# Performance work log

Hardware: AMD Instinct MI355X
Metric: run time of the kernel (lower is better)

## Reference

```python
import jax, jax.numpy as jnp
import numpy as np

D, T1, T2, T3 = 1024, 256, 128, 64
IV2, IV3, BUF = 16, 128, 32
B, T = 16, 1024

_PARAM_SHAPES = {
    "w_t1g": (D + T1, T1), "b_t1g": (T1,),
    "w_t1c": (D + T1, T1), "b_t1c": (T1,),
    "w_t1r": (T1, D), "b_t1r": (D,),
    "w_t2v": (D, T2), "b_t2v": (T2,),
    "w_t2b": (D, 1), "b_t2b": (1,),
    "w_t2r": (T2, D), "b_t2r": (D,),
    "w_t3o": (D, T3), "b_t3o": (T3,),
    "w_t3n": (D, T3), "b_t3n": (T3,),
    "w_t3r": (2 * T3, D), "b_t3r": (D,),
    "w_b32": (T3, T2), "b_b32": (T2,),
    "w_b21": (T2, T1), "b_b21": (T1,),
    "w_fuse": (3 * D, D), "b_fuse": (D,),
}

def setup_inputs() -> dict:
    key = jax.random.key(0)
    inp = {"x": jax.random.normal(jax.random.fold_in(key, 0), (B, T, D), jnp.float32)}
    for i, (name, shape) in enumerate(_PARAM_SHAPES.items()):
        inp[name] = 0.02 * jax.random.normal(jax.random.fold_in(key, i + 1), shape, jnp.float32)
    inp["ln_g"] = jnp.ones((D,), jnp.float32)
    inp["ln_b"] = jnp.zeros((D,), jnp.float32)
    return inp

def reference(x, w_t1g, b_t1g, w_t1c, b_t1c, w_t1r, b_t1r, w_t2v, b_t2v, w_t2b, b_t2b, w_t2r, b_t2r, w_t3o, b_t3o, w_t3n, b_t3n, w_t3r, b_t3r, w_b32, b_b32, w_b21, b_b21, w_fuse, b_fuse, ln_g, ln_b):
    Bsz, Tlen, _ = x.shape
    tier1 = jnp.zeros((Bsz, T1), x.dtype)
    tier2 = jnp.zeros((Bsz, T2), x.dtype)
    tier3 = jnp.zeros((Bsz, T3), x.dtype)
    var3 = jnp.ones((Bsz, T3), x.dtype)
    buf = jnp.zeros((Bsz, BUF, D), x.dtype)  # consolidation buffer

    def step(carry, inp_t):
        tier1, tier2, tier3, var3, buf = carry
        x_t, tc = inp_t  # tc = token_count (1-indexed)
        # cross-tier broadcasts
        bias21 = jnp.tanh(tier2 @ w_b21 + b_b21)
        bias32 = jnp.tanh(tier3 @ w_b32 + b_b32)
        # tier1: GRU-style gated update
        t1b = tier1 + bias21
        comb = jnp.concatenate([x_t, t1b], axis=-1)
        gate = jax.nn.sigmoid(comb @ w_t1g + b_t1g)
        cand = jnp.tanh(comb @ w_t1c + b_t1c)
        tier1 = gate * t1b + (1.0 - gate) * cand
        read1 = tier1 @ w_t1r + b_t1r
        # tier2: delta-rule overwrite every IV2 tokens (buffer mean BEFORE this token is written)
        do2 = (tc % IV2) == 0
        bm = buf.mean(axis=1)
        t2b = tier2 + bias32
        v = bm @ w_t2v + b_t2v
        beta = jax.nn.sigmoid(bm @ w_t2b + b_t2b)
        tier2 = jnp.where(do2, t2b + beta * (v - t2b), tier2)
        read2 = tier2 @ w_t2r + b_t2r
        # tier3: diagonal Kalman update every IV3 tokens, observation = tier2 readout
        do3 = (tc % IV3) == 0
        z = read2 @ w_t3o + b_t3o
        r = jax.nn.softplus(read2 @ w_t3n + b_t3n) + 0.01
        sp = 0.99 * var3 + 0.01
        K = sp / (sp + r + 1e-8)
        tier3 = jnp.where(do3, tier3 + K * (z - tier3), tier3)
        var3 = jnp.where(do3, (1.0 - K) * sp, var3)
        read3 = jnp.concatenate([tier3, var3], axis=-1) @ w_t3r + b_t3r
        fused = jnp.concatenate([read1, read2, read3], axis=-1) @ w_fuse + b_fuse
        # ring-buffer write (detached in torch -> stop_gradient)
        idx = (tc - 1) % BUF
        buf = jax.lax.dynamic_update_slice(buf, jax.lax.stop_gradient(x_t)[:, None, :], (0, idx, 0))
        return (tier1, tier2, tier3, var3, buf), fused

    tcs = jnp.arange(1, Tlen + 1, dtype=jnp.int32)
    _, ys = jax.lax.scan(step, (tier1, tier2, tier3, var3, buf), (jnp.swapaxes(x, 0, 1), tcs))
    out = jnp.swapaxes(ys, 0, 1)  # [B, T, D]
    mu = out.mean(-1, keepdims=True)
    xc = out - mu
    return xc * jax.lax.rsqrt(jnp.mean(xc * xc, -1, keepdims=True) + 1e-5) * ln_g + ln_b
```

## Files before the change

### kernel.cpp

```cpp
#include <hip/hip_runtime.h>

#define D_ 1024
#define T_ 1024
#define B_ 16

typedef short s16x8 __attribute__((ext_vector_type(8)));
typedef float f32x4 __attribute__((ext_vector_type(4)));

__device__ __forceinline__ unsigned short bf16_rne(float f){
  unsigned int u = __builtin_bit_cast(unsigned int, f);
  u += 0x7FFFu + ((u >> 16) & 1u);
  return (unsigned short)(u >> 16);
}
__device__ __forceinline__ float bf16_tof(unsigned short h){
  unsigned int u = ((unsigned int)h) << 16;
  return __builtin_bit_cast(float, u);
}
__device__ __forceinline__ float fsig(float x){ return 1.0f/(1.0f+__expf(-x)); }
__device__ __forceinline__ float ftanh(float x){ return 2.0f*fsig(2.0f*x)-1.0f; }

template <typename V>
__device__ __forceinline__ auto mfma_try(V a, V b, f32x4 c, int)
    -> decltype(__builtin_amdgcn_mfma_f32_16x16x32_bf16(a, b, c, 0, 0, 0)) {
  return __builtin_amdgcn_mfma_f32_16x16x32_bf16(a, b, c, 0, 0, 0);
}
template <typename V>
__device__ __forceinline__ f32x4 mfma_try(V a, V b, f32x4 c, long) {
  typedef __bf16 bf16x8 __attribute__((ext_vector_type(8)));
  return __builtin_amdgcn_mfma_f32_16x16x32_bf16(
      __builtin_bit_cast(bf16x8, a), __builtin_bit_cast(bf16x8, b), c, 0, 0, 0);
}
__device__ __forceinline__ f32x4 MFMA(s16x8 a, s16x8 b, f32x4 c){
  return mfma_try(a, b, c, 0);
}


__device__ __forceinline__ void dev_conv4(const float* __restrict__ s,
                                          unsigned short* __restrict__ d, int g){
  float4 v = *(const float4*)(s + (size_t)g*4);
  ushort4 o; o.x=bf16_rne(v.x); o.y=bf16_rne(v.y); o.z=bf16_rne(v.z); o.w=bf16_rne(v.w);
  *(ushort4*)(d + (size_t)g*4) = o;
}

__device__ __forceinline__ void dev_fragprep(const float* __restrict__ w, int rowOff,
                                             int KT, int Nsrc,
                                             unsigned short* __restrict__ dst, int slot){
  int lane = slot & 63; int tmp = slot >> 6; int kt = tmp % KT; int nt = tmp / KT;
  int kbase = kt*32 + (lane>>4)*8; int col = nt*16 + (lane&15);
  unsigned short* o = dst + (size_t)slot*8;
  #pragma unroll
  for (int j=0;j<8;j++) o[j] = bf16_rne(w[(size_t)(rowOff + kbase + j)*Nsrc + col]);
}

__device__ __forceinline__ void dev_bm(const float* __restrict__ x,
                                       unsigned short* __restrict__ bm, int blk, int tid){
  int e = blk >> 4; int b = blk & 15;
  int tc = 16*(e+1); int hi = tc-2; int lo = tc-33; if (lo < 0) lo = 0;
  const float* xb = x + (size_t)b*T_*D_;
  for (int d = tid; d < D_; d += 256){
    float s = 0.f;
    for (int ss = lo; ss <= hi; ++ss) s += xb[(size_t)ss*D_ + d];
    bm[((size_t)(e*16+b))*D_ + d] = bf16_rne(s * (1.0f/32.0f));
  }
}

__device__ __forceinline__ void dev_bconst(const float* __restrict__ wf, const float* __restrict__ bf,
                                           const float* __restrict__ b1, const float* __restrict__ b2,
                                           const float* __restrict__ b3, float* __restrict__ bc,
                                           int blk, int tid){
  __shared__ float part[4][64];
  int n = blk*64 + (tid&63);
  int sl = tid>>6;
  float s = 0.f;
  for (int k=sl*256; k<(sl+1)*256; ++k){
    s += b1[k]*wf[(size_t)k*1024+n] + b2[k]*wf[(size_t)(1024+k)*1024+n] + b3[k]*wf[(size_t)(2048+k)*1024+n];
  }
  part[sl][tid&63] = s; __syncthreads();
  if (sl==0) bc[n] = bf[n] + part[0][tid] + part[1][tid] + part[2][tid] + part[3][tid];
}

__device__ __forceinline__ void dev_b2(const float* __restrict__ b_t2r, const float* __restrict__ w3o,
                                       const float* __restrict__ b3o, const float* __restrict__ w3n,
                                       const float* __restrict__ b3n, float* __restrict__ b2o,
                                       float* __restrict__ b2n, int tid){
  __shared__ float part[2][128];
  int idx = tid & 127; int sl = tid >> 7;
  int mat = idx>>6, n = idx&63;
  const float* w = mat ? w3n : w3o;
  float s = 0.f;
  for (int k=sl*512; k<(sl+1)*512; ++k) s += b_t2r[k]*w[(size_t)k*64+n];
  part[sl][idx] = s; __syncthreads();
  if (sl==0){
    float r = part[0][idx] + part[1][idx] + (mat? b3n[n] : b3o[n]);
    if (mat) b2n[n] = r; else b2o[n] = r;
  }
}

__device__ __forceinline__ void dev_gemm(int M, int K,
    const unsigned short* __restrict__ A, int lda,
    const unsigned short* __restrict__ Bf,
    const float* __restrict__ bias, int act,
    float* __restrict__ C, int ldc, int cb, int rb, int tid, int rows){
  int KT = K >> 5;
  int w = tid >> 6, l = tid & 63;
  int rbase = rb*rows + w*16;
  int arow = rbase + (l & 15); if (arow >= M) arow = M-1;
  const unsigned short* Aptr = A + (size_t)arow*lda + ((l>>4)*8);
  const s16x8* B0 = (const s16x8*)Bf + ((size_t)(cb*4+0)*KT)*64 + l;
  const s16x8* B1 = (const s16x8*)Bf + ((size_t)(cb*4+1)*KT)*64 + l;
  const s16x8* B2 = (const s16x8*)Bf + ((size_t)(cb*4+2)*KT)*64 + l;
  const s16x8* B3 = (const s16x8*)Bf + ((size_t)(cb*4+3)*KT)*64 + l;
  f32x4 z = {0.f,0.f,0.f,0.f};
  f32x4 acc0=z, acc1=z, acc2=z, acc3=z;
  for (int kt=0; kt<KT; ++kt){
    s16x8 a = *(const s16x8*)(Aptr + (size_t)kt*32);
    acc0 = MFMA(a, B0[(size_t)kt*64], acc0);
    acc1 = MFMA(a, B1[(size_t)kt*64], acc1);
    acc2 = MFMA(a, B2[(size_t)kt*64], acc2);
    acc3 = MFMA(a, B3[(size_t)kt*64], acc3);
  }
  int r0 = (l>>4)*4;
  #pragma unroll
  for (int i=0;i<4;i++){
    f32x4 acc = i==0?acc0 : i==1?acc1 : i==2?acc2 : acc3;
    int col = (cb*4+i)*16 + (l&15);
    float bs = bias ? bias[col] : 0.0f;
    #pragma unroll
    for (int j=0;j<4;j++){
      int row = rbase + r0 + j;
      if (row < M){
        float vv = acc[j] + bs;
        if (act==1) vv = ftanh(vv);
        C[(size_t)row*ldc + col] = vv;
      }
    }
  }
}

__device__ void dev_traj(
    const float* __restrict__ v, const float* __restrict__ beta,
    const float* __restrict__ w_b32, const float* __restrict__ b_b32,
    const float* __restrict__ w2o, const float* __restrict__ b2o,
    const float* __restrict__ w2n, const float* __restrict__ b2n,
    unsigned short* __restrict__ t2traj, unsigned short* __restrict__ t3traj, int tid){
  __shared__ float t2[16*128];
  __shared__ float t3[16*64];
  __shared__ float var3[16*64];
  __shared__ float zb[16*64];
  __shared__ float rb[16*64];
  __shared__ float b32[16*128];
  for (int i=tid;i<2048;i+=1024){ t2[i]=0.f; t2traj[i]=0; }
  for (int i=tid;i<1024;i+=1024){
    int b=i>>6, n=i&63;
    t3[i]=0.f; var3[i]=1.f;
    t3traj[(size_t)b*128 + n] = 0;
    t3traj[(size_t)b*128 + 64 + n] = bf16_rne(1.f);
  }
  __syncthreads();
  for (int g=0; g<8; ++g){
    for (int i=tid;i<2048;i+=1024){
      int b=i>>7, n=i&127;
      float s=b_b32[n];
      for (int j=0;j<64;j++) s += t3[b*64+j]*w_b32[j*128+n];
      b32[i] = ftanh(s);
    }
    __syncthreads();
    for (int kk=0; kk<8; ++kk){
      int k = g*8 + kk + 1;
      for (int i=tid;i<2048;i+=1024){
        int b=i>>7, n=i&127;
        float t2b = t2[i] + b32[i];
        float bt = beta[(k-1)*16+b];
        float nv = t2b + bt*(v[(size_t)((k-1)*16+b)*128+n] - t2b);
        t2[i]=nv;
        t2traj[((size_t)k*16+b)*128+n] = bf16_rne(nv);
      }
    }
    __syncthreads();
    for (int i=tid;i<2048;i+=1024){
      int mat=i>>10, b=(i>>6)&15, n=i&63;
      const float* w = mat? w2n : w2o;
      float s = mat? b2n[n] : b2o[n];
      for (int j=0;j<128;j++) s += t2[b*128+j]*w[j*64+n];
      if (mat){ float r = (s>20.f)? s : log1pf(__expf(s)); rb[b*64+n]=r+0.01f; }
      else zb[b*64+n]=s;
    }
    __syncthreads();
    for (int i=tid;i<1024;i+=1024){
      int b=i>>6, n=i&63;
      float sp = 0.99f*var3[i]+0.01f;
      float Kk = sp/(sp+rb[i]+1e-8f);
      float t3n_ = t3[i] + Kk*(zb[i]-t3[i]);
      float v3n = (1.f-Kk)*sp;
      t3[i]=t3n_; var3[i]=v3n;
      t3traj[((size_t)(g+1)*16+b)*128+n]    = bf16_rne(t3n_);
      t3traj[((size_t)(g+1)*16+b)*128+64+n] = bf16_rne(v3n);
    }
    __syncthreads();
  }
}


__global__ __launch_bounds__(256) void k_f1(
    const float* __restrict__ x, unsigned short* __restrict__ xtb,
    const float* __restrict__ w_t1r, unsigned short* __restrict__ w_t1r_bf,
    const float* __restrict__ w_t2r, unsigned short* __restrict__ w_t2r_bf,
    const float* __restrict__ w_t3r, unsigned short* __restrict__ w_t3r_bf,
    const float* __restrict__ w_t1g, const float* __restrict__ w_t1c,
    unsigned short* __restrict__ wgc1f, unsigned short* __restrict__ wg2f,
    unsigned short* __restrict__ wc2f,
    const float* __restrict__ w_t2v, unsigned short* __restrict__ wtvf,
    const float* __restrict__ w_b21, unsigned short* __restrict__ wb21f,
    const float* __restrict__ w_fuse, unsigned short* __restrict__ wf1f,
    unsigned short* __restrict__ wf2f, unsigned short* __restrict__ wf3f,
    const float* __restrict__ w_t3o, unsigned short* __restrict__ w3of,
    const float* __restrict__ w_t3n, unsigned short* __restrict__ w3nf,
    unsigned short* __restrict__ bm,
    const float* __restrict__ b_fuse, const float* __restrict__ b_t1r,
    const float* __restrict__ b_t2r, const float* __restrict__ b_t3r,
    float* __restrict__ bconst,
    const float* __restrict__ b_t3o, const float* __restrict__ b_t3n,
    float* __restrict__ b2o, float* __restrict__ b2n,
    const float* __restrict__ b_t1g, const float* __restrict__ b_t1c,
    float* __restrict__ bgc){
  int blk = blockIdx.x, tid = threadIdx.x;
  if (blk < 1024){
    for (int i=0;i<16;i++){
      int r = blk*16 + i; int b = r & 15, t = r >> 4; int d = tid*4;
      float4 v = *(const float4*)(x + ((size_t)b*T_ + t)*D_ + d);
      ushort4 o; o.x=bf16_rne(v.x); o.y=bf16_rne(v.y); o.z=bf16_rne(v.z); o.w=bf16_rne(v.w);
      *(ushort4*)(xtb + (size_t)r*D_ + d) = o;
    }
  } else if (blk < 1280){ dev_conv4(w_t1r, w_t1r_bf, (blk-1024)*256 + tid); }
  else if (blk < 1408){ dev_conv4(w_t2r, w_t2r_bf, (blk-1280)*256 + tid); }
  else if (blk < 1536){ dev_conv4(w_t3r, w_t3r_bf, (blk-1408)*256 + tid); }
  else if (blk < 1664){ dev_fragprep(w_t1g, 0, 32, 256, wgc1f,          (blk-1536)*256 + tid); }
  else if (blk < 1792){ dev_fragprep(w_t1c, 0, 32, 256, wgc1f + 262144, (blk-1664)*256 + tid); }
  else if (blk < 1824){ dev_fragprep(w_t1g, 1024, 8, 256, wg2f, (blk-1792)*256 + tid); }
  else if (blk < 1856){ dev_fragprep(w_t1c, 1024, 8, 256, wc2f, (blk-1824)*256 + tid); }
  else if (blk < 1920){ dev_fragprep(w_t2v, 0, 32, 128, wtvf, (blk-1856)*256 + tid); }
  else if (blk < 1936){ dev_fragprep(w_b21, 0, 4, 256, wb21f, (blk-1920)*256 + tid); }
  else if (blk < 2448){ dev_fragprep(w_fuse, 0,    32, 1024, wf1f, (blk-1936)*256 + tid); }
  else if (blk < 2960){ dev_fragprep(w_fuse, 1024, 32, 1024, wf2f, (blk-2448)*256 + tid); }
  else if (blk < 3472){ dev_fragprep(w_fuse, 2048, 32, 1024, wf3f, (blk-2960)*256 + tid); }
  else if (blk < 3504){ dev_fragprep(w_t3o, 0, 32, 64, w3of, (blk-3472)*256 + tid); }
  else if (blk < 3536){ dev_fragprep(w_t3n, 0, 32, 64, w3nf, (blk-3504)*256 + tid); }
  else if (blk < 4560){ dev_bm(x, bm, blk-3536, tid); }
  else if (blk < 4576){ dev_bconst(w_fuse, b_fuse, b_t1r, b_t2r, b_t3r, bconst, blk-4560, tid); }
  else if (blk < 4577){ dev_b2(b_t2r, w_t3o, b_t3o, w_t3n, b_t3n, b2o, b2n, tid); }
  else { bgc[tid] = b_t1g[tid]; bgc[256+tid] = b_t1c[tid]; }
}

__global__ __launch_bounds__(256) void k_f2(
    const unsigned short* __restrict__ xtb, const unsigned short* __restrict__ wgc1f,
    const float* __restrict__ bgc, float* __restrict__ P,
    const unsigned short* __restrict__ bm, const unsigned short* __restrict__ wtvf,
    const float* __restrict__ b_t2v, float* __restrict__ v,
    const unsigned short* __restrict__ w_t1r_bf, const unsigned short* __restrict__ wf1f,
    float* __restrict__ wr1f,
    const unsigned short* __restrict__ w_t2r_bf, const unsigned short* __restrict__ wf2f,
    float* __restrict__ wr2f,
    const unsigned short* __restrict__ w_t3r_bf, const unsigned short* __restrict__ wf3f,
    float* __restrict__ wr3f,
    const unsigned short* __restrict__ w3of, float* __restrict__ w2o,
    const unsigned short* __restrict__ w3nf, float* __restrict__ w2n,
    const float* __restrict__ w_t2b, const float* __restrict__ b_t2b,
    float* __restrict__ beta){
  int blk = blockIdx.x, tid = threadIdx.x;
  if (blk < 2048){ int r = blk;        dev_gemm(16384, 1024, xtb, 1024, wgc1f, bgc, 0, P, 512, r&7, r>>3, tid, 64); }
  else if (blk < 2080){ int r = blk-2048; dev_gemm(1024, 1024, bm, 1024, wtvf, b_t2v, 0, v, 128, r&1, r>>1, tid, 64); }
  else if (blk < 2144){ int r = blk-2080; dev_gemm(256, 1024, w_t1r_bf, 1024, wf1f, nullptr, 0, wr1f, 1024, r&15, r>>4, tid, 64); }
  else if (blk < 2176){ int r = blk-2144; dev_gemm(128, 1024, w_t2r_bf, 1024, wf2f, nullptr, 0, wr2f, 1024, r&15, r>>4, tid, 64); }
  else if (blk < 2208){ int r = blk-2176; dev_gemm(128, 1024, w_t3r_bf, 1024, wf3f, nullptr, 0, wr3f, 1024, r&15, r>>4, tid, 64); }
  else if (blk < 2210){ int r = blk-2208; dev_gemm(128, 1024, w_t2r_bf, 1024, w3of, nullptr, 0, w2o, 64, 0, r, tid, 64); }
  else if (blk < 2212){ int r = blk-2210; dev_gemm(128, 1024, w_t2r_bf, 1024, w3nf, nullptr, 0, w2n, 64, 0, r, tid, 64); }
  else {
    int rel = blk-2212;
    int r = rel*4 + (tid>>6), l = tid&63;
    float s = 0.f;
    for (int d=l; d<D_; d+=64) s += bf16_tof(bm[(size_t)r*D_+d]) * w_t2b[d];
    #pragma unroll
    for (int off=32; off; off>>=1) s += __shfl_down(s, off);
    if (l==0) beta[r] = fsig(s + b_t2b[0]);
  }
}

__global__ __launch_bounds__(1024) void k_f3(
    const float* __restrict__ wr1f, unsigned short* __restrict__ wr1ff,
    const float* __restrict__ wr2f, unsigned short* __restrict__ wr2ff,
    const float* __restrict__ wr3f, unsigned short* __restrict__ wr3ff,
    const float* __restrict__ v, const float* __restrict__ beta,
    const float* __restrict__ w_b32, const float* __restrict__ b_b32,
    const float* __restrict__ w2o, const float* __restrict__ b2o,
    const float* __restrict__ w2n, const float* __restrict__ b2n,
    unsigned short* __restrict__ t2traj, unsigned short* __restrict__ t3traj){
  int blk = blockIdx.x, tid = threadIdx.x;
  if (blk < 32){ dev_fragprep(wr1f, 0, 8, 1024, wr1ff, blk*1024 + tid); }
  else if (blk < 48){ dev_fragprep(wr2f, 0, 4, 1024, wr2ff, (blk-32)*1024 + tid); }
  else if (blk < 64){ dev_fragprep(wr3f, 0, 4, 1024, wr3ff, (blk-48)*1024 + tid); }
  else { dev_traj(v, beta, w_b32, b_b32, w2o, b2o, w2n, b2n, t2traj, t3traj, tid); }
}

__global__ __launch_bounds__(256) void k_f4(
    const unsigned short* __restrict__ t2traj, const unsigned short* __restrict__ wb21f,
    const float* __restrict__ b_b21, float* __restrict__ b21seg){
  int blk = blockIdx.x, tid = threadIdx.x;
  dev_gemm(1040, 128, t2traj, 128, wb21f, b_b21, 1, b21seg, 256, blk&3, blk>>2, tid, 64);
}

__global__ __launch_bounds__(1024, 1) void k_recur(
    const float* __restrict__ P,
    const float* __restrict__ b21,
    const unsigned short* __restrict__ Wg2f, const unsigned short* __restrict__ Wc2f,
    unsigned short* __restrict__ traj,
    const unsigned short* __restrict__ t2traj, const unsigned short* __restrict__ wr2ff,
    float* __restrict__ f2seg,
    const unsigned short* __restrict__ t3traj, const unsigned short* __restrict__ wr3ff,
    float* __restrict__ f3seg){
  __shared__ unsigned short sbuf[2][256];
  int blk = blockIdx.x, tid = threadIdx.x;
  if (blk >= 16){
    int rel = blk - 16;
    if (rel < 80) dev_gemm(1040, 128, t2traj, 128, wr2ff, nullptr, 0, f2seg, 1024, rel&15, rel>>4, tid, 256);
    else          dev_gemm(144,  128, t3traj, 128, wr3ff, nullptr, 0, f3seg, 1024, rel-80, 0,     tid, 256);
    return;
  }
  int b = blk;
  int w = tid>>6, l = tid&63;
  int hi = l>>4, cl = l&15;
  const s16x8* Bg = (const s16x8*)Wg2f;
  const s16x8* Bc = (const s16x8*)Wc2f;
  s16x8 bg[8], bc[8];
  #pragma unroll
  for (int kt=0;kt<8;kt++){
    bg[kt] = Bg[((size_t)(w*8+kt))*64 + l];
    bc[kt] = Bc[((size_t)(w*8+kt))*64 + l];
  }
  bool owner = (hi == 0);
  int n = w*16 + cl;
  float t1b = 0.f;
  float pgN=0.f, pcN=0.f, bbN=0.f;
  if (owner){
    bbN = b21[((size_t)b)*256 + n];
    t1b = bbN;
    pgN = P[((size_t)b)*512 + n];
    pcN = P[((size_t)b)*512 + 256 + n];
    sbuf[0][n] = bf16_rne(t1b);
  }
  asm volatile("s_waitcnt lgkmcnt(0)\ns_barrier" ::: "memory");
  for (int t=0;t<1024;t++){
    float pg = pgN, pc = pcN, bb = bbN;
    int tn = (t+1 < 1024) ? (t+1) : 1023;
    if (owner){
      pgN = P[((size_t)(tn*16+b))*512 + n];
      pcN = P[((size_t)(tn*16+b))*512 + 256 + n];
      bbN = b21[(((size_t)((t+2)>>4))*16 + b)*256 + n];
    }
    const unsigned short* sb = sbuf[t&1];
    f32x4 z = {0.f,0.f,0.f,0.f};
    f32x4 ag=z, ac=z;
    #pragma unroll
    for (int kt=0;kt<8;kt++){
      s16x8 a = *(const s16x8*)(sb + kt*32 + hi*8);
      ag = MFMA(a, bg[kt], ag);
      ac = MFMA(a, bc[kt], ac);
    }
    if (owner){
      float g = fsig(ag[0] + pg);
      float c = ftanh(ac[0] + pc);
      float t1n = g*t1b + (1.f-g)*c;
      traj[((size_t)(t*16+b))*256 + n] = bf16_rne(t1n);
      t1b = t1n + bb;
      sbuf[(t+1)&1][n] = bf16_rne(t1b);
    }
    asm volatile("s_waitcnt lgkmcnt(0)\ns_barrier" ::: "memory");
  }
}

__global__ __launch_bounds__(1024) void k_final(
    const unsigned short* __restrict__ traj, const unsigned short* __restrict__ Bf,
    const float* __restrict__ bconst, const float* __restrict__ f2seg, const float* __restrict__ f3seg,
    const float* __restrict__ ln_g, const float* __restrict__ ln_b, float* __restrict__ out){
  __shared__ float buf[16*1024];
  __shared__ float mu[16];
  __shared__ float rs[16];
  int t = blockIdx.x, tid = threadIdx.x, w = tid>>6, l = tid&63;
  const unsigned short* Ab = traj + ((size_t)t*16 + (l&15))*256 + (l>>4)*8;
  const s16x8* Bp = (const s16x8*)Bf;
  f32x4 z = {0.f,0.f,0.f,0.f};
  f32x4 ac[4]; ac[0]=z; ac[1]=z; ac[2]=z; ac[3]=z;
  #pragma unroll
  for (int kt=0;kt<8;kt++){
    s16x8 a = *(const s16x8*)(Ab + kt*32);
    #pragma unroll
    for (int i=0;i<4;i++){
      int nt = w*4+i;
      ac[i] = MFMA(a, Bp[((size_t)nt*8+kt)*64+l], ac[i]);
    }
  }
  int tc = t+1, s2 = tc>>4, s3 = tc>>7;
  int r0 = (l>>4)*4, cl = l&15;
  #pragma unroll
  for (int i=0;i<4;i++){
    int col = (w*4+i)*16+cl;
    #pragma unroll
    for (int j=0;j<4;j++){
      int b = r0+j;
      buf[b*1024+col] = ac[i][j] + bconst[col]
        + f2seg[((size_t)s2*16+b)*1024+col] + f3seg[((size_t)s3*16+b)*1024+col];
    }
  }
  __syncthreads();
  {
    float s=0.f, q=0.f;
    #pragma unroll
    for (int i=0;i<16;i++){ float xv = buf[w*1024 + l + 64*i]; s+=xv; q+=xv*xv; }
    #pragma unroll
    for (int off=32;off;off>>=1){ s += __shfl_down(s,off); q += __shfl_down(q,off); }
    if (l==0){ float m = s*(1.f/1024.f); float var = q*(1.f/1024.f) - m*m; mu[w]=m; rs[w]=rsqrtf(var+1e-5f); }
  }
  __syncthreads();
  {
    int b = tid>>6, d0 = tid&63;
    float m = mu[b], r = rs[b];
    size_t ob = ((size_t)b*1024 + t)*1024;
    #pragma unroll
    for (int i=0;i<16;i++){
      int d = d0 + 64*i;
      out[ob + d] = (buf[b*1024+d]-m)*r*ln_g[d] + ln_b[d];
    }
  }
}

extern "C" void kernel_launch(void* const* d_in, const int* in_sizes, int n_in,
                              void* d_out, int out_size, void* d_ws, size_t ws_size,
                              hipStream_t stream){
  const float* x     = (const float*)d_in[0];
  const float* w_t1g = (const float*)d_in[1];
  const float* b_t1g = (const float*)d_in[2];
  const float* w_t1c = (const float*)d_in[3];
  const float* b_t1c = (const float*)d_in[4];
  const float* w_t1r = (const float*)d_in[5];
  const float* b_t1r = (const float*)d_in[6];
  const float* w_t2v = (const float*)d_in[7];
  const float* b_t2v = (const float*)d_in[8];
  const float* w_t2b = (const float*)d_in[9];
  const float* b_t2b = (const float*)d_in[10];
  const float* w_t2r = (const float*)d_in[11];
  const float* b_t2r = (const float*)d_in[12];
  const float* w_t3o = (const float*)d_in[13];
  const float* b_t3o = (const float*)d_in[14];
  const float* w_t3n = (const float*)d_in[15];
  const float* b_t3n = (const float*)d_in[16];
  const float* w_t3r = (const float*)d_in[17];
  const float* b_t3r = (const float*)d_in[18];
  const float* w_b32 = (const float*)d_in[19];
  const float* b_b32 = (const float*)d_in[20];
  const float* w_b21 = (const float*)d_in[21];
  const float* b_b21 = (const float*)d_in[22];
  const float* w_fuse= (const float*)d_in[23];
  const float* b_fuse= (const float*)d_in[24];
  const float* ln_g  = (const float*)d_in[25];
  const float* ln_b  = (const float*)d_in[26];
  float* out = (float*)d_out;
  (void)in_sizes; (void)n_in; (void)out_size; (void)ws_size;

  char* base = (char*)d_ws;
  size_t off = 0;
  auto alloc = [&](size_t bytes) -> void* {
    void* p = base + off;
    off += (bytes + 255) & ~(size_t)255;
    return p;
  };
  unsigned short* xtb   = (unsigned short*)alloc((size_t)B_*T_*D_*2);
  float* P              = (float*)alloc((size_t)B_*T_*512*4);
  unsigned short* traj1 = (unsigned short*)alloc((size_t)B_*T_*256*2);
  unsigned short* bm    = (unsigned short*)alloc((size_t)1024*1024*2);
  float* v      = (float*)alloc((size_t)1024*128*4);
  float* beta   = (float*)alloc(1024*4);
  float* wr1f   = (float*)alloc((size_t)256*1024*4);
  float* wr2f   = (float*)alloc((size_t)128*1024*4);
  float* wr3f   = (float*)alloc((size_t)128*1024*4);
  float* w2o    = (float*)alloc(128*64*4);
  float* w2n    = (float*)alloc(128*64*4);
  float* b2o    = (float*)alloc(64*4);
  float* b2n    = (float*)alloc(64*4);
  float* bconst = (float*)alloc(1024*4);
  float* bgc    = (float*)alloc(512*4);
  unsigned short* t2traj = (unsigned short*)alloc((size_t)1040*128*2);
  unsigned short* t3traj = (unsigned short*)alloc((size_t)144*128*2);
  float* b21seg = (float*)alloc((size_t)1040*256*4);
  float* f2seg  = (float*)alloc((size_t)1040*1024*4);
  float* f3seg  = (float*)alloc((size_t)144*1024*4);
  unsigned short* w_t1r_bf = (unsigned short*)alloc((size_t)256*1024*2);
  unsigned short* w_t2r_bf = (unsigned short*)alloc((size_t)128*1024*2);
  unsigned short* w_t3r_bf = (unsigned short*)alloc((size_t)128*1024*2);
  unsigned short* wgc1f = (unsigned short*)alloc((size_t)1024*512*2);
  unsigned short* wg2f  = (unsigned short*)alloc((size_t)256*256*2);
  unsigned short* wc2f  = (unsigned short*)alloc((size_t)256*256*2);
  unsigned short* wtvf  = (unsigned short*)alloc((size_t)1024*128*2);
  unsigned short* wb21f = (unsigned short*)alloc((size_t)128*256*2);
  unsigned short* wf1f  = (unsigned short*)alloc((size_t)1024*1024*2);
  unsigned short* wf2f  = (unsigned short*)alloc((size_t)1024*1024*2);
  unsigned short* wf3f  = (unsigned short*)alloc((size_t)1024*1024*2);
  unsigned short* w3of  = (unsigned short*)alloc((size_t)1024*64*2);
  unsigned short* w3nf  = (unsigned short*)alloc((size_t)1024*64*2);
  unsigned short* wr1ff = (unsigned short*)alloc((size_t)256*1024*2);
  unsigned short* wr2ff = (unsigned short*)alloc((size_t)128*1024*2);
  unsigned short* wr3ff = (unsigned short*)alloc((size_t)128*1024*2);

  k_f1<<<dim3(4578), dim3(256), 0, stream>>>(
      x, xtb, w_t1r, w_t1r_bf, w_t2r, w_t2r_bf, w_t3r, w_t3r_bf,
      w_t1g, w_t1c, wgc1f, wg2f, wc2f, w_t2v, wtvf, w_b21, wb21f,
      w_fuse, wf1f, wf2f, wf3f, w_t3o, w3of, w_t3n, w3nf, bm,
      b_fuse, b_t1r, b_t2r, b_t3r, bconst, b_t3o, b_t3n, b2o, b2n,
      b_t1g, b_t1c, bgc);
  k_f2<<<dim3(2468), dim3(256), 0, stream>>>(
      xtb, wgc1f, bgc, P, bm, wtvf, b_t2v, v,
      w_t1r_bf, wf1f, wr1f, w_t2r_bf, wf2f, wr2f, w_t3r_bf, wf3f, wr3f,
      w3of, w2o, w3nf, w2n, w_t2b, b_t2b, beta);
  k_f3<<<dim3(65), dim3(1024), 0, stream>>>(
      wr1f, wr1ff, wr2f, wr2ff, wr3f, wr3ff,
      v, beta, w_b32, b_b32, w2o, b2o, w2n, b2n, t2traj, t3traj);
  k_f4<<<dim3(68), dim3(256), 0, stream>>>(t2traj, wb21f, b_b21, b21seg);
  k_recur<<<dim3(112), dim3(1024), 0, stream>>>(
      P, b21seg, wg2f, wc2f, traj1,
      t2traj, wr2ff, f2seg, t3traj, wr3ff, f3seg);
  k_final<<<dim3(1024), dim3(1024), 0, stream>>>(traj1, wr1ff, bconst, f2seg, f3seg, ln_g, ln_b, out);
}
```

Measured before the change: 1.137 ms.

## Halve recurrence block width, widen P GEMM tiles, fold b21 GEMM into traj kernel

The sequential tier-1 recurrence now runs with 512 threads per batch block, and each wave owns two 16-column tiles with four MFMAs per k step. This is meant to cut barrier cost per timestep, and the blocks running side-work GEMMs are resized to match. The input-projection GEMM uses a new kernel that computes 8 column tiles per block, raising A-operand reuse and halving the block count. The separate k_f4 launch is removed: the b21 GEMM runs inside the trajectory block after a __syncthreads, which saves one launch but serializes that GEMM onto a single block.

New measurement: 1.166 ms. 1.03x slower.

```diff
diff --git a/kernel.cpp b/kernel.cpp
--- a/kernel.cpp
+++ b/kernel.cpp
@@ -133,6 +133,37 @@
         if (act==1) vv = ftanh(vv);
         C[(size_t)row*ldc + col] = vv;
       }
+    }
+  }
+}
+
+__device__ __forceinline__ void dev_gemm8_P(
+    const unsigned short* __restrict__ A, const unsigned short* __restrict__ Bf,
+    const float* __restrict__ bias, float* __restrict__ C,
+    int cbp, int rb, int tid){
+  int w = tid >> 6, l = tid & 63;
+  int rbase = rb*64 + w*16;
+  int arow = rbase + (l & 15);
+  const unsigned short* Aptr = A + (size_t)arow*1024 + ((l>>4)*8);
+  const s16x8* Bbase = (const s16x8*)Bf;
+  f32x4 z = {0.f,0.f,0.f,0.f};
+  f32x4 acc[8];
+  #pragma unroll
+  for (int i=0;i<8;i++) acc[i]=z;
+  for (int kt=0; kt<32; ++kt){
+    s16x8 a = *(const s16x8*)(Aptr + (size_t)kt*32);
+    #pragma unroll
+    for (int i=0;i<8;i++)
+      acc[i] = MFMA(a, Bbase[((size_t)(cbp*8+i)*32 + kt)*64 + l], acc[i]);
+  }
+  int r0 = (l>>4)*4;
+  #pragma unroll
+  for (int i=0;i<8;i++){
+    int col = (cbp*8+i)*16 + (l&15);
+    float bs = bias[col];
+    #pragma unroll
+    for (int j=0;j<4;j++){
+      C[(size_t)(rbase + r0 + j)*512 + col] = acc[i][j] + bs;
     }
   }
 }
@@ -267,15 +298,15 @@
     const float* __restrict__ w_t2b, const float* __restrict__ b_t2b,
     float* __restrict__ beta){
   int blk = blockIdx.x, tid = threadIdx.x;
-  if (blk < 2048){ int r = blk;        dev_gemm(16384, 1024, xtb, 1024, wgc1f, bgc, 0, P, 512, r&7, r>>3, tid, 64); }
-  else if (blk < 2080){ int r = blk-2048; dev_gemm(1024, 1024, bm, 1024, wtvf, b_t2v, 0, v, 128, r&1, r>>1, tid, 64); }
-  else if (blk < 2144){ int r = blk-2080; dev_gemm(256, 1024, w_t1r_bf, 1024, wf1f, nullptr, 0, wr1f, 1024, r&15, r>>4, tid, 64); }
-  else if (blk < 2176){ int r = blk-2144; dev_gemm(128, 1024, w_t2r_bf, 1024, wf2f, nullptr, 0, wr2f, 1024, r&15, r>>4, tid, 64); }
-  else if (blk < 2208){ int r = blk-2176; dev_gemm(128, 1024, w_t3r_bf, 1024, wf3f, nullptr, 0, wr3f, 1024, r&15, r>>4, tid, 64); }
-  else if (blk < 2210){ int r = blk-2208; dev_gemm(128, 1024, w_t2r_bf, 1024, w3of, nullptr, 0, w2o, 64, 0, r, tid, 64); }
-  else if (blk < 2212){ int r = blk-2210; dev_gemm(128, 1024, w_t2r_bf, 1024, w3nf, nullptr, 0, w2n, 64, 0, r, tid, 64); }
+  if (blk < 1024){ int r = blk;        dev_gemm8_P(xtb, wgc1f, bgc, P, r&3, r>>2, tid); }
+  else if (blk < 1056){ int r = blk-1024; dev_gemm(1024, 1024, bm, 1024, wtvf, b_t2v, 0, v, 128, r&1, r>>1, tid, 64); }
+  else if (blk < 1120){ int r = blk-1056; dev_gemm(256, 1024, w_t1r_bf, 1024, wf1f, nullptr, 0, wr1f, 1024, r&15, r>>4, tid, 64); }
+  else if (blk < 1152){ int r = blk-1120; dev_gemm(128, 1024, w_t2r_bf, 1024, wf2f, nullptr, 0, wr2f, 1024, r&15, r>>4, tid, 64); }
+  else if (blk < 1184){ int r = blk-1152; dev_gemm(128, 1024, w_t3r_bf, 1024, wf3f, nullptr, 0, wr3f, 1024, r&15, r>>4, tid, 64); }
+  else if (blk < 1186){ int r = blk-1184; dev_gemm(128, 1024, w_t2r_bf, 1024, w3of, nullptr, 0, w2o, 64, 0, r, tid, 64); }
+  else if (blk < 1188){ int r = blk-1186; dev_gemm(128, 1024, w_t2r_bf, 1024, w3nf, nullptr, 0, w2n, 64, 0, r, tid, 64); }
   else {
-    int rel = blk-2212;
+    int rel = blk-1188;
     int r = rel*4 + (tid>>6), l = tid&63;
     float s = 0.f;
     for (int d=l; d<D_; d+=64) s += bf16_tof(bm[(size_t)r*D_+d]) * w_t2b[d];
@@ -293,22 +324,23 @@
     const float* __restrict__ w_b32, const float* __restrict__ b_b32,
     const float* __restrict__ w2o, const float* __restrict__ b2o,
     const float* __restrict__ w2n, const float* __restrict__ b2n,
-    unsigned short* __restrict__ t2traj, unsigned short* __restrict__ t3traj){
+    unsigned short* __restrict__ t2traj, unsigned short* __restrict__ t3traj,
+    const unsigned short* __restrict__ wb21f, const float* __restrict__ b_b21,
+    float* __restrict__ b21seg){
   int blk = blockIdx.x, tid = threadIdx.x;
   if (blk < 32){ dev_fragprep(wr1f, 0, 8, 1024, wr1ff, blk*1024 + tid); }
   else if (blk < 48){ dev_fragprep(wr2f, 0, 4, 1024, wr2ff, (blk-32)*1024 + tid); }
   else if (blk < 64){ dev_fragprep(wr3f, 0, 4, 1024, wr3ff, (blk-48)*1024 + tid); }
-  else { dev_traj(v, beta, w_b32, b_b32, w2o, b2o, w2n, b2n, t2traj, t3traj, tid); }
-}
-
-__global__ __launch_bounds__(256) void k_f4(
-    const unsigned short* __restrict__ t2traj, const unsigned short* __restrict__ wb21f,
-    const float* __restrict__ b_b21, float* __restrict__ b21seg){
-  int blk = blockIdx.x, tid = threadIdx.x;
-  dev_gemm(1040, 128, t2traj, 128, wb21f, b_b21, 1, b21seg, 256, blk&3, blk>>2, tid, 64);
-}
-
-__global__ __launch_bounds__(1024, 1) void k_recur(
+  else {
+    dev_traj(v, beta, w_b32, b_b32, w2o, b2o, w2n, b2n, t2traj, t3traj, tid);
+    __syncthreads();
+    int sb = tid >> 8, stid = tid & 255;
+    for (int vb = sb; vb < 68; vb += 4)
+      dev_gemm(1040, 128, t2traj, 128, wb21f, b_b21, 1, b21seg, 256, vb&3, vb>>2, stid, 64);
+  }
+}
+
+__global__ __launch_bounds__(512) void k_recur(
     const float* __restrict__ P,
     const float* __restrict__ b21,
     const unsigned short* __restrict__ Wg2f, const unsigned short* __restrict__ Wc2f,
@@ -321,8 +353,9 @@
   int blk = blockIdx.x, tid = threadIdx.x;
   if (blk >= 16){
     int rel = blk - 16;
-    if (rel < 80) dev_gemm(1040, 128, t2traj, 128, wr2ff, nullptr, 0, f2seg, 1024, rel&15, rel>>4, tid, 256);
-    else          dev_gemm(144,  128, t3traj, 128, wr3ff, nullptr, 0, f3seg, 1024, rel-80, 0,     tid, 256);
+    if (rel < 144) dev_gemm(1040, 128, t2traj, 128, wr2ff, nullptr, 0, f2seg, 1024, rel&15, rel>>4, tid, 128);
+    else { rel -= 144;
+           dev_gemm(144,  128, t3traj, 128, wr3ff, nullptr, 0, f3seg, 1024, rel&15, rel>>4, tid, 128); }
     return;
   }
   int b = blk;
@@ -330,14 +363,18 @@
   int hi = l>>4, cl = l&15;
   const s16x8* Bg = (const s16x8*)Wg2f;
   const s16x8* Bc = (const s16x8*)Wc2f;
-  s16x8 bg[8], bc[8];
+  s16x8 bg0[8], bg1[8], bc0[8], bc1[8];
   #pragma unroll
   for (int kt=0;kt<8;kt++){
-    bg[kt] = Bg[((size_t)(w*8+kt))*64 + l];
-    bc[kt] = Bc[((size_t)(w*8+kt))*64 + l];
-  }
-  bool owner = (hi == 0);
-  int n = w*16 + cl;
+    bg0[kt] = Bg[((size_t)(2*w)*8  +kt)*64 + l];
+    bg1[kt] = Bg[((size_t)(2*w+1)*8+kt)*64 + l];
+    bc0[kt] = Bc[((size_t)(2*w)*8  +kt)*64 + l];
+    bc1[kt] = Bc[((size_t)(2*w+1)*8+kt)*64 + l];
+  }
+  bool owner = (hi < 2);
+  int nt = 2*w + hi;
+  int n  = nt*16 + cl;
+  if (!owner) n = 2*w*16 + cl;
   float t1b = 0.f;
   float pgN=0.f, pcN=0.f, bbN=0.f;
   if (owner){
@@ -358,16 +395,20 @@
     }
     const unsigned short* sb = sbuf[t&1];
     f32x4 z = {0.f,0.f,0.f,0.f};
-    f32x4 ag=z, ac=z;
+    f32x4 ag0=z, ag1=z, ac0=z, ac1=z;
     #pragma unroll
     for (int kt=0;kt<8;kt++){
       s16x8 a = *(const s16x8*)(sb + kt*32 + hi*8);
-      ag = MFMA(a, bg[kt], ag);
-      ac = MFMA(a, bc[kt], ac);
+      ag0 = MFMA(a, bg0[kt], ag0);
+      ag1 = MFMA(a, bg1[kt], ag1);
+      ac0 = MFMA(a, bc0[kt], ac0);
+      ac1 = MFMA(a, bc1[kt], ac1);
     }
     if (owner){
-      float g = fsig(ag[0] + pg);
-      float c = ftanh(ac[0] + pc);
+      float gacc = (hi==0)? ag0[0] : ag1[0];
+      float cacc = (hi==0)? ac0[0] : ac1[0];
+      float g = fsig(gacc + pg);
+      float c = ftanh(cacc + pc);
       float t1n = g*t1b + (1.f-g)*c;
       traj[((size_t)(t*16+b))*256 + n] = bf16_rne(t1n);
       t1b = t1n + bb;
@@ -515,15 +556,15 @@
       w_fuse, wf1f, wf2f, wf3f, w_t3o, w3of, w_t3n, w3nf, bm,
       b_fuse, b_t1r, b_t2r, b_t3r, bconst, b_t3o, b_t3n, b2o, b2n,
       b_t1g, b_t1c, bgc);
-  k_f2<<<dim3(2468), dim3(256), 0, stream>>>(
+  k_f2<<<dim3(1444), dim3(256), 0, stream>>>(
       xtb, wgc1f, bgc, P, bm, wtvf, b_t2v, v,
       w_t1r_bf, wf1f, wr1f, w_t2r_bf, wf2f, wr2f, w_t3r_bf, wf3f, wr3f,
       w3of, w2o, w3nf, w2n, w_t2b, b_t2b, beta);
   k_f3<<<dim3(65), dim3(1024), 0, stream>>>(
       wr1f, wr1ff, wr2f, wr2ff, wr3f, wr3ff,
-      v, beta, w_b32, b_b32, w2o, b2o, w2n, b2n, t2traj, t3traj);
-  k_f4<<<dim3(68), dim3(256), 0, stream>>>(t2traj, wb21f, b_b21, b21seg);
-  k_recur<<<dim3(112), dim3(1024), 0, stream>>>(
+      v, beta, w_b32, b_b32, w2o, b2o, w2n, b2n, t2traj, t3traj,
+      wb21f, b_b21, b21seg);
+  k_recur<<<dim3(192), dim3(512), 0, stream>>>(
       P, b21seg, wg2f, wc2f, traj1,
       t2traj, wr2ff, f2seg, t3traj, wr3ff, f3seg);
   k_final<<<dim3(1024), dim3(1024), 0, stream>>>(traj1, wr1ff, bconst, f2seg, f3seg, ln_g, ln_b, out);
```

## Halve recurrence block to 512 threads with two N-tiles per wave

Applied to the files above, without the earlier changes.

The serial tier-1 recurrence kernel now runs with 8 waves per batch block instead of 16. Each wave computes two 16-column tiles of the gate and candidate MFMAs, and lanes in the second row group own the second tile. Fewer waves per block should make the per-step barrier cheaper, at the cost of twice the MFMA work and register-held weights per wave. The side GEMM blocks that overlap the recurrence are re-split into more blocks with 128 threads each, which changes the grid to 192 blocks.

After: 1.101 ms, median of 6. 3.2% less time.

```diff
diff --git a/kernel.cpp b/kernel.cpp
--- a/kernel.cpp
+++ b/kernel.cpp
@@ -308,7 +308,7 @@
   dev_gemm(1040, 128, t2traj, 128, wb21f, b_b21, 1, b21seg, 256, blk&3, blk>>2, tid, 64);
 }
 
-__global__ __launch_bounds__(1024, 1) void k_recur(
+__global__ __launch_bounds__(512) void k_recur(
     const float* __restrict__ P,
     const float* __restrict__ b21,
     const unsigned short* __restrict__ Wg2f, const unsigned short* __restrict__ Wc2f,
@@ -321,8 +321,9 @@
   int blk = blockIdx.x, tid = threadIdx.x;
   if (blk >= 16){
     int rel = blk - 16;
-    if (rel < 80) dev_gemm(1040, 128, t2traj, 128, wr2ff, nullptr, 0, f2seg, 1024, rel&15, rel>>4, tid, 256);
-    else          dev_gemm(144,  128, t3traj, 128, wr3ff, nullptr, 0, f3seg, 1024, rel-80, 0,     tid, 256);
+    if (rel < 144) dev_gemm(1040, 128, t2traj, 128, wr2ff, nullptr, 0, f2seg, 1024, rel&15, rel>>4, tid, 128);
+    else { rel -= 144;
+           dev_gemm(144,  128, t3traj, 128, wr3ff, nullptr, 0, f3seg, 1024, rel&15, rel>>4, tid, 128); }
     return;
   }
   int b = blk;
@@ -330,14 +331,18 @@
   int hi = l>>4, cl = l&15;
   const s16x8* Bg = (const s16x8*)Wg2f;
   const s16x8* Bc = (const s16x8*)Wc2f;
-  s16x8 bg[8], bc[8];
+  s16x8 bg0[8], bg1[8], bc0[8], bc1[8];
   #pragma unroll
   for (int kt=0;kt<8;kt++){
-    bg[kt] = Bg[((size_t)(w*8+kt))*64 + l];
-    bc[kt] = Bc[((size_t)(w*8+kt))*64 + l];
-  }
-  bool owner = (hi == 0);
-  int n = w*16 + cl;
+    bg0[kt] = Bg[((size_t)(2*w)*8  +kt)*64 + l];
+    bg1[kt] = Bg[((size_t)(2*w+1)*8+kt)*64 + l];
+    bc0[kt] = Bc[((size_t)(2*w)*8  +kt)*64 + l];
+    bc1[kt] = Bc[((size_t)(2*w+1)*8+kt)*64 + l];
+  }
+  bool owner = (hi < 2);
+  int nt = 2*w + hi;
+  int n  = nt*16 + cl;
+  if (!owner) n = 2*w*16 + cl;
   float t1b = 0.f;
   float pgN=0.f, pcN=0.f, bbN=0.f;
   if (owner){
@@ -358,16 +363,20 @@
     }
     const unsigned short* sb = sbuf[t&1];
     f32x4 z = {0.f,0.f,0.f,0.f};
-    f32x4 ag=z, ac=z;
+    f32x4 ag0=z, ag1=z, ac0=z, ac1=z;
     #pragma unroll
     for (int kt=0;kt<8;kt++){
       s16x8 a = *(const s16x8*)(sb + kt*32 + hi*8);
-      ag = MFMA(a, bg[kt], ag);
-      ac = MFMA(a, bc[kt], ac);
+      ag0 = MFMA(a, bg0[kt], ag0);
+      ag1 = MFMA(a, bg1[kt], ag1);
+      ac0 = MFMA(a, bc0[kt], ac0);
+      ac1 = MFMA(a, bc1[kt], ac1);
     }
     if (owner){
-      float g = fsig(ag[0] + pg);
-      float c = ftanh(ac[0] + pc);
+      float gacc = (hi==0)? ag0[0] : ag1[0];
+      float cacc = (hi==0)? ac0[0] : ac1[0];
+      float g = fsig(gacc + pg);
+      float c = ftanh(cacc + pc);
       float t1n = g*t1b + (1.f-g)*c;
       traj[((size_t)(t*16+b))*256 + n] = bf16_rne(t1n);
       t1b = t1n + bb;
@@ -523,7 +532,7 @@
       wr1f, wr1ff, wr2f, wr2ff, wr3f, wr3ff,
       v, beta, w_b32, b_b32, w2o, b2o, w2n, b2n, t2traj, t3traj);
   k_f4<<<dim3(68), dim3(256), 0, stream>>>(t2traj, wb21f, b_b21, b21seg);
-  k_recur<<<dim3(112), dim3(1024), 0, stream>>>(
+  k_recur<<<dim3(192), dim3(512), 0, stream>>>(
       P, b21seg, wg2f, wc2f, traj1,
       t2traj, wr2ff, f2seg, t3traj, wr3ff, f3seg);
   k_final<<<dim3(1024), dim3(1024), 0, stream>>>(traj1, wr1ff, bconst, f2seg, f3seg, ln_g, ln_b, out);
```
